# Optimization experiments

Hardware: AMD Instinct MI355X
Metric: run time of the kernel (lower is better)

## Reference

```python
import jax, jax.numpy as jnp
import numpy as np

NEG_SLOPE = 0.2  # PyG GATConv default negative_slope


def gat_layer(x, W, a_src, a_dst, b, src, dst, N):
    # x: [N, Fin], W: [Fin, H*C], a_src/a_dst: [H, C], b: [C]
    H, C = a_src.shape
    h = (x @ W).reshape(N, H, C)
    # per-node attention halves
    s = (h * a_src).sum(-1)  # [N, H]
    d = (h * a_dst).sum(-1)  # [N, H]
    e = jax.nn.leaky_relu(s[src] + d[dst], NEG_SLOPE)  # [E, H]
    # segment softmax over destination nodes (every node has a self-loop)
    m = jax.ops.segment_max(e, dst, num_segments=N)
    ex = jnp.exp(e - m[dst])
    denom = jax.ops.segment_sum(ex, dst, num_segments=N)
    alpha = ex / denom[dst]  # [E, H]
    out = jax.ops.segment_sum(h[src] * alpha[:, :, None], dst, num_segments=N)  # [N, H, C]
    return out.mean(axis=1) + b  # head-averaged output [N, C]


def setup_inputs() -> dict:
    key = jax.random.key(0)
    ks = jax.random.split(key, 16)
    N, E, D, H, C = 50000, 800000, 128, 2, 64
    inp = {
        "X": jax.random.normal(ks[0], (N, D), dtype=jnp.float32),
        "edge_index": jax.random.randint(ks[1], (2, E), 0, N, dtype=jnp.int64),
        "edge_weight": jax.random.uniform(ks[2], (E,), dtype=jnp.float32),
    }
    dims = [D, C, C, C]
    for i in range(3):
        fin = dims[i]
        inp[f"W{i+1}"] = jax.random.normal(ks[3 + 4 * i], (fin, H * C), dtype=jnp.float32) * 0.1
        inp[f"a_src{i+1}"] = jax.random.normal(ks[4 + 4 * i], (H, C), dtype=jnp.float32) * 0.1
        inp[f"a_dst{i+1}"] = jax.random.normal(ks[5 + 4 * i], (H, C), dtype=jnp.float32) * 0.1
        inp[f"b{i+1}"] = jnp.zeros((C,), dtype=jnp.float32)
    inp["Wl"] = jax.random.normal(ks[15], (C, 1), dtype=jnp.float32) * 0.1
    inp["bl"] = jnp.zeros((1,), dtype=jnp.float32)
    return inp


def reference(X, edge_index, edge_weight, W1, a_src1, a_dst1, b1,
              W2, a_src2, a_dst2, b2, W3, a_src3, a_dst3, b3, Wl, bl):
    N = X.shape[0]
    loops = jnp.arange(N, dtype=edge_index.dtype)  # add_self_loops=True default
    src = jnp.concatenate([edge_index[0], loops])
    dst = jnp.concatenate([edge_index[1], loops])
    x = jax.nn.elu(gat_layer(X, W1, a_src1, a_dst1, b1, src, dst, N))
    x = jax.nn.elu(gat_layer(x, W2, a_src2, a_dst2, b2, src, dst, N))
    x = jax.nn.elu(gat_layer(x, W3, a_src3, a_dst3, b3, src, dst, N))
    logit = x @ Wl + bl  # [N, 1]
    return jax.nn.sigmoid(logit)[:, 0]
```

## Files before the change

kernel.cpp:

```cpp
#include <hip/hip_runtime.h>
#include <math.h>

#define NEG_SLOPE 0.2f
#define ESHIFT 8.0f

__device__ __forceinline__ float lrelu(float x) { return x > 0.f ? x : NEG_SLOPE * x; }
__device__ __forceinline__ int clampi(int v, int n) { return min(max(v, 0), n - 1); }
__device__ __forceinline__ unsigned f2bf(float f) {
    unsigned u = __float_as_uint(f);
    return (u + 0x7fffu + ((u >> 16) & 1u)) >> 16;
}


__global__ void hist(const int* __restrict__ ei, int* __restrict__ deg, int E, int N) {
    const int i = blockIdx.x * blockDim.x + threadIdx.x;
    if (i >= E) return;
    atomicAdd(&deg[clampi(ei[E + i], N)], 1);
}

__global__ void scan_partial(const int* __restrict__ deg, int* __restrict__ off,
                             int* __restrict__ bsum, int N) {
    __shared__ int wsum[16];
    const int tid = threadIdx.x, lane = tid & 63, wid = tid >> 6;
    const int i = blockIdx.x * 1024 + tid;
    const int v = (i < N) ? deg[i] : 0;
    int x = v;
#pragma unroll
    for (int o = 1; o < 64; o <<= 1) { int y = __shfl_up(x, o); if (lane >= o) x += y; }
    if (lane == 63) wsum[wid] = x;
    __syncthreads();
    if (wid == 0) {
        int ws = (lane < 16) ? wsum[lane] : 0;
#pragma unroll
        for (int o = 1; o < 16; o <<= 1) { int y = __shfl_up(ws, o); if (lane >= o) ws += y; }
        if (lane < 16) wsum[lane] = ws;
    }
    __syncthreads();
    const int wp = wid ? wsum[wid - 1] : 0;
    if (i < N) off[i] = wp + x - v;
    if (tid == 0) bsum[blockIdx.x] = wsum[15];
}

__global__ void scan_bsums(int* __restrict__ bsum, int nb) {
    const int lane = threadIdx.x;
    int carry = 0;
    for (int base = 0; base < nb; base += 64) {
        const int i = base + lane;
        const int v = (i < nb) ? bsum[i] : 0;
        int x = v;
#pragma unroll
        for (int o = 1; o < 64; o <<= 1) { int y = __shfl_up(x, o); if (lane >= o) x += y; }
        if (i < nb) bsum[i] = carry + x - v;
        carry += __shfl(x, 63);
    }
}

__global__ void scan_add(int* __restrict__ off, const int* __restrict__ bsum, int N) {
    const int i = blockIdx.x * 1024 + threadIdx.x;
    if (i < N) off[i] += bsum[blockIdx.x];
}

__global__ void scatter(const int* __restrict__ ei, int* __restrict__ off,
                        int* __restrict__ csr, int E, int N) {
    const int i = blockIdx.x * blockDim.x + threadIdx.x;
    if (i >= E) return;
    const int src = clampi(ei[i], N);
    const int dst = clampi(ei[E + i], N);
    csr[atomicAdd(&off[dst], 1)] = src;
}


template <int FIN>
__global__ __launch_bounds__(256) void gemm_sd(
        const float* __restrict__ x, const float* __restrict__ W,
        const float* __restrict__ a_src, const float* __restrict__ a_dst,
        unsigned* __restrict__ hb, float* __restrict__ s, float* __restrict__ d, int N) {
    __shared__ float xs[64 * FIN];
    const int tid = threadIdx.x;
    const int nb = blockIdx.x * 64;
    const int nrows = min(64, N - nb);
    for (int i = tid * 4; i < nrows * FIN; i += 1024)
        *(float4*)&xs[i] = *(const float4*)&x[(size_t)nb * FIN + i];
    __syncthreads();

    const int cg = (tid & 31) * 4;
    const int ng = tid >> 5;
    float acc[8][4];
#pragma unroll
    for (int i = 0; i < 8; ++i)
#pragma unroll
        for (int j = 0; j < 4; ++j) acc[i][j] = 0.f;

#pragma unroll 2
    for (int k = 0; k < FIN; ++k) {
        const float4 wv = *(const float4*)&W[k * 128 + cg];
#pragma unroll
        for (int i = 0; i < 8; ++i) {
            const float xv = xs[(ng + 8 * i) * FIN + k];
            acc[i][0] = fmaf(xv, wv.x, acc[i][0]);
            acc[i][1] = fmaf(xv, wv.y, acc[i][1]);
            acc[i][2] = fmaf(xv, wv.z, acc[i][2]);
            acc[i][3] = fmaf(xv, wv.w, acc[i][3]);
        }
    }

    const int head = cg >> 6;
    const int c0 = cg & 63;
    const float4 asv = *(const float4*)&a_src[head * 64 + c0];
    const float4 adv = *(const float4*)&a_dst[head * 64 + c0];
#pragma unroll
    for (int i = 0; i < 8; ++i) {
        const int n = nb + ng + 8 * i;
        if (n < N) {
            hb[(size_t)n * 64 + (cg >> 1) + 0] = f2bf(acc[i][0]) | (f2bf(acc[i][1]) << 16);
            hb[(size_t)n * 64 + (cg >> 1) + 1] = f2bf(acc[i][2]) | (f2bf(acc[i][3]) << 16);
        }
        float ps = acc[i][0] * asv.x + acc[i][1] * asv.y + acc[i][2] * asv.z + acc[i][3] * asv.w;
        float pd = acc[i][0] * adv.x + acc[i][1] * adv.y + acc[i][2] * adv.z + acc[i][3] * adv.w;
#pragma unroll
        for (int o = 1; o < 16; o <<= 1) {
            ps += __shfl_xor(ps, o);
            pd += __shfl_xor(pd, o);
        }
        if ((tid & 15) == 0 && n < N) {
            s[n * 2 + head] = ps;
            d[n * 2 + head] = pd;
        }
    }
}

template <bool FINAL>
__global__ void aggregate(const int* __restrict__ csr, const int* __restrict__ offend,
                          const int* __restrict__ deg, const unsigned* __restrict__ hb,
                          const float* __restrict__ s, const float* __restrict__ d,
                          const float* __restrict__ b, float* __restrict__ xout,
                          const float* __restrict__ Wl, const float* __restrict__ bl,
                          float* __restrict__ out, int N) {
    const int lane = threadIdx.x & 63;
    const int n = blockIdx.x * (blockDim.x >> 6) + (threadIdx.x >> 6);
    if (n >= N) return;
    const float2 dn = *(const float2*)&d[2 * n];
    const float2 sn = *(const float2*)&s[2 * n];
    const float exs0 = __expf(lrelu(sn.x + dn.x) - ESHIFT);
    const float exs1 = __expf(lrelu(sn.y + dn.y) - ESHIFT);
    const unsigned us = hb[(size_t)n * 64 + lane];
    const float wself = (lane < 32) ? exs0 : exs1;
    float ax = wself * __uint_as_float(us << 16);
    float ay = wself * __uint_as_float(us & 0xffff0000u);
    float den0 = (lane == 0) ? exs0 : 0.f;
    float den1 = (lane == 0) ? exs1 : 0.f;

    const int cnt = deg[n];
    const int start = offend[n] - cnt;
    for (int base = 0; base < cnt; base += 64) {
        const int cc = min(cnt - base, 64);
        int srcl = n;
        float ex0 = 0.f, ex1 = 0.f;
        if (lane < cc) {
            srcl = csr[start + base + lane];
            const float2 ss = *(const float2*)&s[2 * srcl];
            ex0 = __expf(lrelu(ss.x + dn.x) - ESHIFT);
            ex1 = __expf(lrelu(ss.y + dn.y) - ESHIFT);
        }
        den0 += ex0;
        den1 += ex1;
        const int rnd = (cc + 3) & ~3;
        for (int j = 0; j < rnd; j += 4) {
#pragma unroll
            for (int t = 0; t < 4; ++t) {
                const int sj = __shfl(srcl, j + t);
                const float w0 = __shfl(ex0, j + t);
                const float w1 = __shfl(ex1, j + t);
                const float w = (lane < 32) ? w0 : w1;
                const unsigned u = hb[(size_t)sj * 64 + lane];
                ax = fmaf(w, __uint_as_float(u << 16), ax);
                ay = fmaf(w, __uint_as_float(u & 0xffff0000u), ay);
            }
        }
    }
#pragma unroll
    for (int o = 32; o; o >>= 1) {
        den0 += __shfl_xor(den0, o);
        den1 += __shfl_xor(den1, o);
    }
    const float dsel = (lane < 32) ? den0 : den1;
    const float tx = ax / dsel, ty = ay / dsel;
    const float ox = __shfl_xor(tx, 32), oy = __shfl_xor(ty, 32);
    const int c0 = (lane & 31) * 2;
    const float2 bb = *(const float2*)&b[c0];
    float vx = 0.5f * (tx + ox) + bb.x;
    float vy = 0.5f * (ty + oy) + bb.y;
    vx = vx > 0.f ? vx : expm1f(vx);
    vy = vy > 0.f ? vy : expm1f(vy);
    if (!FINAL) {
        if (lane < 32) *(float2*)&xout[(size_t)n * 64 + c0] = make_float2(vx, vy);
    } else {
        const float2 wl = *(const float2*)&Wl[c0];
        float t = (lane < 32) ? (vx * wl.x + vy * wl.y) : 0.f;
#pragma unroll
        for (int o = 32; o; o >>= 1) t += __shfl_down(t, o);
        if (lane == 0) out[n] = 1.f / (1.f + expf(-(t + bl[0])));
    }
}

extern "C" void kernel_launch(void* const* d_in, const int* in_sizes, int n_in,
                              void* d_out, int out_size, void* d_ws, size_t ws_size,
                              hipStream_t stream) {
    const float* X = (const float*)d_in[0];
    const int* ei = (const int*)d_in[1];
    const float* Wm[3] = {(const float*)d_in[3], (const float*)d_in[7], (const float*)d_in[11]};
    const float* As[3] = {(const float*)d_in[4], (const float*)d_in[8], (const float*)d_in[12]};
    const float* Ad[3] = {(const float*)d_in[5], (const float*)d_in[9], (const float*)d_in[13]};
    const float* Bs[3] = {(const float*)d_in[6], (const float*)d_in[10], (const float*)d_in[14]};
    const float* Wl = (const float*)d_in[15];
    const float* bl = (const float*)d_in[16];
    float* out = (float*)d_out;

    const int N = in_sizes[0] / 128;
    const int E = in_sizes[1] / 2;
    const int nb = (N + 1023) / 1024;

    char* w = (char*)d_ws;
    unsigned* hb = (unsigned*)w; w += (size_t)N * 64 * sizeof(unsigned);
    float* xb = (float*)w;       w += (size_t)N * 64 * sizeof(float);
    float* sA = (float*)w;       w += (size_t)N * 2 * sizeof(float);
    float* dA = (float*)w;       w += (size_t)N * 2 * sizeof(float);
    int* deg = (int*)w;          w += (size_t)N * sizeof(int);
    int* off = (int*)w;          w += (size_t)N * sizeof(int);
    int* bsum = (int*)w;         w += (size_t)(nb + 1) * sizeof(int);
    int* csr = (int*)w;          w += (size_t)E * sizeof(int);

    hipMemsetAsync(deg, 0, (size_t)N * sizeof(int), stream);
    hist<<<(E + 255) / 256, 256, 0, stream>>>(ei, deg, E, N);
    scan_partial<<<nb, 1024, 0, stream>>>(deg, off, bsum, N);
    scan_bsums<<<1, 64, 0, stream>>>(bsum, nb);
    scan_add<<<nb, 1024, 0, stream>>>(off, bsum, N);
    scatter<<<(E + 255) / 256, 256, 0, stream>>>(ei, off, csr, E, N);

    const float* xin = X;
    const int gblk = (N + 63) / 64;
    for (int L = 0; L < 3; ++L) {
        if (L == 0)
            gemm_sd<128><<<gblk, 256, 0, stream>>>(xin, Wm[L], As[L], Ad[L], hb, sA, dA, N);
        else
            gemm_sd<64><<<gblk, 256, 0, stream>>>(xin, Wm[L], As[L], Ad[L], hb, sA, dA, N);
        if (L < 2) {
            aggregate<false><<<(N + 3) / 4, 256, 0, stream>>>(csr, off, deg, hb, sA, dA, Bs[L],
                                                              xb, nullptr, nullptr, nullptr, N);
            xin = xb;
        } else {
            aggregate<true><<<(N + 3) / 4, 256, 0, stream>>>(csr, off, deg, hb, sA, dA, Bs[L],
                                                             nullptr, Wl, bl, out, N);
        }
    }
}
```

Measured before the change: 394.3 us.

## Replace three-pass scan with atomic bucket allocation and deepen GEMM/aggregate unrolling

```diff
diff --git a/kernel.cpp b/kernel.cpp
--- a/kernel.cpp
+++ b/kernel.cpp
@@ -18,9 +18,10 @@
     atomicAdd(&deg[clampi(ei[E + i], N)], 1);
 }
 
-__global__ void scan_partial(const int* __restrict__ deg, int* __restrict__ off,
-                             int* __restrict__ bsum, int N) {
+__global__ void alloc_scan(const int* __restrict__ deg, int* __restrict__ off,
+                           int* __restrict__ total, int N) {
     __shared__ int wsum[16];
+    __shared__ int base_s;
     const int tid = threadIdx.x, lane = tid & 63, wid = tid >> 6;
     const int i = blockIdx.x * 1024 + tid;
     const int v = (i < N) ? deg[i] : 0;
@@ -36,28 +37,10 @@
         if (lane < 16) wsum[lane] = ws;
     }
     __syncthreads();
+    if (tid == 0) base_s = atomicAdd(total, wsum[15]);
+    __syncthreads();
     const int wp = wid ? wsum[wid - 1] : 0;
-    if (i < N) off[i] = wp + x - v;
-    if (tid == 0) bsum[blockIdx.x] = wsum[15];
-}
-
-__global__ void scan_bsums(int* __restrict__ bsum, int nb) {
-    const int lane = threadIdx.x;
-    int carry = 0;
-    for (int base = 0; base < nb; base += 64) {
-        const int i = base + lane;
-        const int v = (i < nb) ? bsum[i] : 0;
-        int x = v;
-#pragma unroll
-        for (int o = 1; o < 64; o <<= 1) { int y = __shfl_up(x, o); if (lane >= o) x += y; }
-        if (i < nb) bsum[i] = carry + x - v;
-        carry += __shfl(x, 63);
-    }
-}
-
-__global__ void scan_add(int* __restrict__ off, const int* __restrict__ bsum, int N) {
-    const int i = blockIdx.x * 1024 + threadIdx.x;
-    if (i < N) off[i] += bsum[blockIdx.x];
+    if (i < N) off[i] = base_s + wp + x - v;
 }
 
 __global__ void scatter(const int* __restrict__ ei, int* __restrict__ off,
@@ -91,16 +74,20 @@
 #pragma unroll
         for (int j = 0; j < 4; ++j) acc[i][j] = 0.f;
 
-#pragma unroll 2
-    for (int k = 0; k < FIN; ++k) {
-        const float4 wv = *(const float4*)&W[k * 128 + cg];
-#pragma unroll
-        for (int i = 0; i < 8; ++i) {
-            const float xv = xs[(ng + 8 * i) * FIN + k];
-            acc[i][0] = fmaf(xv, wv.x, acc[i][0]);
-            acc[i][1] = fmaf(xv, wv.y, acc[i][1]);
-            acc[i][2] = fmaf(xv, wv.z, acc[i][2]);
-            acc[i][3] = fmaf(xv, wv.w, acc[i][3]);
+    for (int k0 = 0; k0 < FIN; k0 += 8) {
+        float4 wv[8];
+#pragma unroll
+        for (int t = 0; t < 8; ++t) wv[t] = *(const float4*)&W[(k0 + t) * 128 + cg];
+#pragma unroll
+        for (int t = 0; t < 8; ++t) {
+#pragma unroll
+            for (int i = 0; i < 8; ++i) {
+                const float xv = xs[(ng + 8 * i) * FIN + k0 + t];
+                acc[i][0] = fmaf(xv, wv[t].x, acc[i][0]);
+                acc[i][1] = fmaf(xv, wv[t].y, acc[i][1]);
+                acc[i][2] = fmaf(xv, wv[t].z, acc[i][2]);
+                acc[i][3] = fmaf(xv, wv[t].w, acc[i][3]);
+            }
         }
     }
 
@@ -164,10 +151,10 @@
         }
         den0 += ex0;
         den1 += ex1;
-        const int rnd = (cc + 3) & ~3;
-        for (int j = 0; j < rnd; j += 4) {
-#pragma unroll
-            for (int t = 0; t < 4; ++t) {
+        const int rnd = (cc + 7) & ~7;
+        for (int j = 0; j < rnd; j += 8) {
+#pragma unroll
+            for (int t = 0; t < 8; ++t) {
                 const int sj = __shfl(srcl, j + t);
                 const float w0 = __shfl(ex0, j + t);
                 const float w1 = __shfl(ex1, j + t);
@@ -225,16 +212,14 @@
     float* xb = (float*)w;       w += (size_t)N * 64 * sizeof(float);
     float* sA = (float*)w;       w += (size_t)N * 2 * sizeof(float);
     float* dA = (float*)w;       w += (size_t)N * 2 * sizeof(float);
-    int* deg = (int*)w;          w += (size_t)N * sizeof(int);
+    int* deg = (int*)w;          w += (size_t)(N + 1) * sizeof(int);
+    int* total = deg + N;
     int* off = (int*)w;          w += (size_t)N * sizeof(int);
-    int* bsum = (int*)w;         w += (size_t)(nb + 1) * sizeof(int);
     int* csr = (int*)w;          w += (size_t)E * sizeof(int);
 
-    hipMemsetAsync(deg, 0, (size_t)N * sizeof(int), stream);
+    hipMemsetAsync(deg, 0, (size_t)(N + 1) * sizeof(int), stream);
     hist<<<(E + 255) / 256, 256, 0, stream>>>(ei, deg, E, N);
-    scan_partial<<<nb, 1024, 0, stream>>>(deg, off, bsum, N);
-    scan_bsums<<<1, 64, 0, stream>>>(bsum, nb);
-    scan_add<<<nb, 1024, 0, stream>>>(off, bsum, N);
+    alloc_scan<<<nb, 1024, 0, stream>>>(deg, off, total, N);
     scatter<<<(E + 255) / 256, 256, 0, stream>>>(ei, off, csr, E, N);
 
     const float* xin = X;
```

Result: no change. 395.5 us (+0.3%).
